# Kernel optimization log

Hardware: AMD Instinct MI355X
Metric: run time of the kernel (lower is better)

Reference implementation:

```python
import jax, jax.numpy as jnp
import numpy as np

N, E, IN_FT, OUT_FT = 8192, 4096, 512, 512
DENSITY = 0.02


def setup_inputs() -> dict:
    key = jax.random.key(0)
    k1, k2, k3, k4 = jax.random.split(key, 4)
    x = jax.random.normal(k1, (N, IN_FT), dtype=jnp.float32)
    hypergraph = (jax.random.uniform(k2, (N, E)) < DENSITY).astype(jnp.float32)
    # kaiming_uniform on [in, out]: fan_in = in_ft (torch fan of a Linear-style 2D param is dim 1 size? torch computes fan_in = size(1) for 2D -> out_ft here)
    bound_w = float(np.sqrt(6.0 / OUT_FT))  # kaiming_uniform a=sqrt(5)? default a=0 -> gain sqrt(2); bound = gain*sqrt(3/fan_in)
    bound_w = float(np.sqrt(2.0) * np.sqrt(3.0 / OUT_FT))
    weight = jax.random.uniform(k3, (IN_FT, OUT_FT), minval=-bound_w, maxval=bound_w, dtype=jnp.float32)
    bound_v = float(np.sqrt(2.0) * np.sqrt(3.0 / 1.0))
    V = jax.random.uniform(k4, (IN_FT, 1), minval=-bound_v, maxval=bound_v, dtype=jnp.float32)
    bias = jnp.zeros((OUT_FT,), dtype=jnp.float32)
    return {"x": x, "hypergraph": hypergraph, "weight": weight, "V": V, "bias": bias}


def reference(x, hypergraph, weight, V, bias):
    # edge embeddings: H^T @ x  -> [E, in_ft]
    edge_emb = hypergraph.T @ x
    hw = jax.nn.sigmoid(edge_emb @ V)          # [E, 1] learned hyperedge weights
    w = hw[:, 0]                                # [E]
    deg_v = (hypergraph @ hw)[:, 0]             # [N]  (sum over last dim of H @ hw)
    deg_e = jnp.sum(hypergraph, axis=0)         # [E]
    # adj = diag(deg_v) @ H @ diag(w) @ diag(deg_e) @ H^T @ diag(deg_v)
    # fused as broadcasted row/col scalings around two GEMMs (same math, no NxN)
    out = x @ weight                            # [N, out_ft]
    t = hypergraph.T @ (deg_v[:, None] * out)   # [E, out_ft]
    t = (w * deg_e)[:, None] * t                # diagonal edge scalings
    out = deg_v[:, None] * (hypergraph @ t)     # [N, out_ft]
    out = out + bias
    return (out, w)
```

## Files before the change

kernel.cpp:

```cpp
#include <hip/hip_runtime.h>


#define N_NODES 8192
#define N_EDGES 4096
#define FT 512

typedef short bf16x8 __attribute__((ext_vector_type(8)));
typedef float f32x4 __attribute__((ext_vector_type(4)));
typedef unsigned short u16;
typedef unsigned int u32;

__device__ __forceinline__ u16 f2b(float f) {
    union { float f; u32 u; } v; v.f = f;
    u32 r = v.u + 0x7FFFu + ((v.u >> 16) & 1u);
    return (u16)(r >> 16);
}
__device__ __forceinline__ float b2f(u16 h) {
    union { u32 u; float f; } v; v.u = ((u32)h) << 16; return v.f;
}


__global__ __launch_bounds__(256) void zero_kernel(float* p, int n) {
    int i = blockIdx.x * 256 + threadIdx.x;
    if (i < n) p[i] = 0.f;
}

__global__ __launch_bounds__(256) void xv_xb_kernel(const float* __restrict__ x,
                                                    const float* __restrict__ V,
                                                    float* __restrict__ xv,
                                                    u16* __restrict__ xb) {
    int row = blockIdx.x * 4 + (threadIdx.x >> 6);
    int lane = threadIdx.x & 63;
    const float* xr = x + (size_t)row * FT + lane * 8;
    const float* vr = V + lane * 8;
    float4 a0 = *(const float4*)xr, a1 = *(const float4*)(xr + 4);
    float4 b0 = *(const float4*)vr, b1 = *(const float4*)(vr + 4);
    float acc = a0.x * b0.x + a0.y * b0.y + a0.z * b0.z + a0.w * b0.w +
                a1.x * b1.x + a1.y * b1.y + a1.z * b1.z + a1.w * b1.w;
    u16 tmp[8] = {f2b(a0.x), f2b(a0.y), f2b(a0.z), f2b(a0.w),
                  f2b(a1.x), f2b(a1.y), f2b(a1.z), f2b(a1.w)};
    *(uint4*)(xb + (size_t)row * FT + lane * 8) = *(uint4*)tmp;
#pragma unroll
    for (int off = 32; off; off >>= 1) acc += __shfl_down(acc, off);
    if (lane == 0) xv[row] = acc;
}

__global__ __launch_bounds__(256) void prep_h2_kernel(const float* __restrict__ H,
                                                      const float* __restrict__ xv,
                                                      u16* __restrict__ Hbf,
                                                      u16* __restrict__ HTbf,
                                                      float* __restrict__ zsum,
                                                      float* __restrict__ desum) {
    __shared__ u32 Wt[64][33];
    __shared__ float xvs[64];
    const int t = threadIdx.x;
    const int e0 = blockIdx.x * 64, n0 = blockIdx.y * 64;
    if (t < 64) xvs[t] = xv[n0 + t];
    {
        int n = t >> 2, seg = t & 3;
        const float* src = H + (size_t)(n0 + n) * N_EDGES + e0 + seg * 16;
        u16* hdst = Hbf + (size_t)(n0 + n) * N_EDGES + e0 + seg * 16;
        u32 o[8];
#pragma unroll
        for (int j = 0; j < 4; j++) {
            float4 h = *(const float4*)(src + j * 4);
            o[2 * j]     = (h.x != 0.f ? 0x3F80u : 0u) | (h.y != 0.f ? 0x3F800000u : 0u);
            o[2 * j + 1] = (h.z != 0.f ? 0x3F80u : 0u) | (h.w != 0.f ? 0x3F800000u : 0u);
        }
        *(uint4*)hdst       = *(uint4*)&o[0];
        *(uint4*)(hdst + 8) = *(uint4*)&o[4];
#pragma unroll
        for (int j = 0; j < 8; j++) Wt[n][seg * 8 + j] = o[j];
    }
    __syncthreads();
    {
        int e = t >> 2, g = t & 3;
        int ew = e >> 1;
        u32 sel = (e & 1) ? 0x07060302u : 0x05040100u;
        u32 oo[8];
        float z = 0.f, d = 0.f;
#pragma unroll
        for (int j = 0; j < 8; j++) {
            int np = g * 8 + j;
            oo[j] = __builtin_amdgcn_perm(Wt[2 * np + 1][ew], Wt[2 * np][ew], sel);
            z += (oo[j] & 0xFFFFu) ? xvs[2 * np] : 0.f;
            d += (oo[j] & 0xFFFFu) ? 1.f : 0.f;
            z += (oo[j] >> 16) ? xvs[2 * np + 1] : 0.f;
            d += (oo[j] >> 16) ? 1.f : 0.f;
        }
        u32* drow = (u32*)(HTbf + (size_t)(e0 + e) * N_NODES + n0);
        *(uint4*)(drow + g * 8)     = *(uint4*)&oo[0];
        *(uint4*)(drow + g * 8 + 4) = *(uint4*)&oo[4];
        z += __shfl_down(z, 2); z += __shfl_down(z, 1);
        d += __shfl_down(d, 2); d += __shfl_down(d, 1);
        if (g == 0) {
            atomicAdd(zsum + e0 + e, z);
            atomicAdd(desum + e0 + e, d);
        }
    }
}

__global__ __launch_bounds__(256) void sigmoid_kernel(const float* __restrict__ zsum,
                                                      const float* __restrict__ desum,
                                                      float* __restrict__ w_out,
                                                      float* __restrict__ wde) {
    int e = blockIdx.x * 256 + threadIdx.x;
    float z = zsum[e];
    float wv = 1.f / (1.f + expf(-z));
    w_out[e] = wv;
    wde[e] = wv * desum[e];
}

__global__ __launch_bounds__(256) void degv_kernel(const u16* __restrict__ Hbf,
                                                   const float* __restrict__ w,
                                                   float* __restrict__ degv) {
    int row = blockIdx.x * 4 + (threadIdx.x >> 6);
    int lane = threadIdx.x & 63;
    const uint4* hr = (const uint4*)(Hbf + (size_t)row * N_EDGES);
    float acc = 0.f;
#pragma unroll
    for (int i = 0; i < 8; i++) {
        int idx = i * 64 + lane;
        uint4 h = hr[idx];
        const float* w8 = w + idx * 8;
        float4 wa = *(const float4*)w8, wb = *(const float4*)(w8 + 4);
        acc += (h.x & 0xFFFFu) ? wa.x : 0.f;  acc += (h.x >> 16) ? wa.y : 0.f;
        acc += (h.y & 0xFFFFu) ? wa.z : 0.f;  acc += (h.y >> 16) ? wa.w : 0.f;
        acc += (h.z & 0xFFFFu) ? wb.x : 0.f;  acc += (h.z >> 16) ? wb.y : 0.f;
        acc += (h.w & 0xFFFFu) ? wb.z : 0.f;  acc += (h.w >> 16) ? wb.w : 0.f;
    }
#pragma unroll
    for (int off = 32; off; off >>= 1) acc += __shfl_down(acc, off);
    if (lane == 0) degv[row] = acc;
}

__global__ void wt_kernel(const float* __restrict__ src, u16* __restrict__ dst) {
    __shared__ float tile[32][33];
    int tx = threadIdx.x, ty = threadIdx.y;
    int c = blockIdx.x * 32 + tx;
    int r0 = blockIdx.y * 32;
#pragma unroll
    for (int i = 0; i < 4; i++)
        tile[ty + i * 8][tx] = src[(size_t)(r0 + ty + i * 8) * FT + c];
    __syncthreads();
#pragma unroll
    for (int i = 0; i < 4; i++)
        dst[(size_t)(blockIdx.x * 32 + ty + i * 8) * FT + r0 + tx] = f2b(tile[tx][ty + i * 8]);
}

__global__ void t2t_kernel(const u16* __restrict__ P, const float* __restrict__ wde,
                           u16* __restrict__ t2T) {
    __shared__ float tile[32][33];
    int tx = threadIdx.x, ty = threadIdx.y;
    int f0 = blockIdx.x * 32, e0 = blockIdx.y * 32;
#pragma unroll
    for (int i = 0; i < 4; i++) {
        int e = e0 + ty + i * 8;
        size_t idx = (size_t)e * 512 + f0 + tx;
        float s = 0.f;
#pragma unroll
        for (int sl = 0; sl < 8; sl++)
            s += b2f(P[idx + (size_t)sl * N_EDGES * 512]);
        tile[ty + i * 8][tx] = wde[e] * s;
    }
    __syncthreads();
#pragma unroll
    for (int i = 0; i < 4; i++)
        t2T[(size_t)(f0 + ty + i * 8) * N_EDGES + e0 + tx] = f2b(tile[tx][ty + i * 8]);
}

__global__ __launch_bounds__(256) void final_kernel(const u16* __restrict__ P,
                                                    const float* __restrict__ degv,
                                                    const float* __restrict__ bias,
                                                    float* __restrict__ out) {
    int i8 = blockIdx.x * 256 + threadIdx.x;
    int base = i8 * 8;
    int n = base >> 9, f = base & 511;
    float s[8] = {0.f, 0.f, 0.f, 0.f, 0.f, 0.f, 0.f, 0.f};
#pragma unroll
    for (int sl = 0; sl < 4; sl++) {
        uint4 v = *(const uint4*)(P + (size_t)sl * N_NODES * 512 + base);
        u32 ws[4] = {v.x, v.y, v.z, v.w};
#pragma unroll
        for (int j = 0; j < 4; j++) {
            s[2 * j]     += b2f((u16)(ws[j] & 0xFFFFu));
            s[2 * j + 1] += b2f((u16)(ws[j] >> 16));
        }
    }
    float dv = degv[n];
    float4 o0, o1;
    o0.x = dv * s[0] + bias[f + 0]; o0.y = dv * s[1] + bias[f + 1];
    o0.z = dv * s[2] + bias[f + 2]; o0.w = dv * s[3] + bias[f + 3];
    o1.x = dv * s[4] + bias[f + 4]; o1.y = dv * s[5] + bias[f + 5];
    o1.z = dv * s[6] + bias[f + 6]; o1.w = dv * s[7] + bias[f + 7];
    *(float4*)(out + base) = o0;
    *(float4*)(out + base + 4) = o1;
}


#define TBK 64

template <int MT, int NT, int EPI>
__global__ __launch_bounds__(256, 4)
void gemm9(const u16* __restrict__ Ap, const u16* __restrict__ Bp,
           void* __restrict__ Cp, const float* __restrict__ degv,
           int KC, int lda, int ldb, int ldc, size_t Ssz) {
    __shared__ __align__(16) u16 Alds[MT * 32 * TBK];
    __shared__ __align__(16) u16 Blds[NT * 32 * TBK];
    const int t = threadIdx.x;
    const int m0 = blockIdx.x * (MT * 32), n0 = blockIdx.y * (NT * 32);
    const int kbase = blockIdx.z * KC;
    const int wave = t >> 6, lane = t & 63, quad = lane >> 4, lo = lane & 15;
    const int wm = (wave >> 1) * (MT * 16), wn = (wave & 1) * (NT * 16);

    f32x4 acc[MT][NT];
#pragma unroll
    for (int a = 0; a < MT; a++)
#pragma unroll
        for (int b = 0; b < NT; b++) acc[a][b] = (f32x4){0.f, 0.f, 0.f, 0.f};

    for (int kk = 0; kk < KC; kk += TBK) {
        const int k0 = kbase + kk;
        __syncthreads();
#pragma unroll
        for (int i = 0; i < MT; i++) {
            int c = t + i * 256;
            int r = c >> 3;
            int j = ((c & 7) - r) & 7;
            const u16* g = Ap + (size_t)(m0 + r) * lda + k0 + j * 8;
            __builtin_amdgcn_global_load_lds((const u32*)g, (u32*)(Alds + c * 8), 16, 0, 0);
        }
#pragma unroll
        for (int i = 0; i < NT; i++) {
            int c = t + i * 256;
            int r = c >> 3;
            int j = ((c & 7) - r) & 7;
            const u16* g = Bp + (size_t)(n0 + r) * ldb + k0 + j * 8;
            __builtin_amdgcn_global_load_lds((const u32*)g, (u32*)(Blds + c * 8), 16, 0, 0);
        }
        __syncthreads();

#pragma unroll
        for (int s2 = 0; s2 < 2; s2++) {
            bf16x8 af[MT], bfr[NT];
#pragma unroll
            for (int mt = 0; mt < MT; mt++) {
                int m = wm + mt * 16 + lo;
                int s = (s2 * 4 + quad + m) & 7;
                af[mt] = *(const bf16x8*)&Alds[m * TBK + s * 8];
            }
#pragma unroll
            for (int nt = 0; nt < NT; nt++) {
                int n = wn + nt * 16 + lo;
                int s = (s2 * 4 + quad + n) & 7;
                bfr[nt] = *(const bf16x8*)&Blds[n * TBK + s * 8];
            }
#pragma unroll
            for (int mt = 0; mt < MT; mt++)
#pragma unroll
                for (int nt = 0; nt < NT; nt++)
                    acc[mt][nt] = __builtin_amdgcn_mfma_f32_16x16x32_bf16(af[mt], bfr[nt], acc[mt][nt], 0, 0, 0);
        }
    }

    if (EPI == 0) {
        u16* C = (u16*)Cp + (size_t)blockIdx.z * Ssz;
#pragma unroll
        for (int mt = 0; mt < MT; mt++) {
            int rb = m0 + wm + mt * 16 + quad * 4;
#pragma unroll
            for (int i = 0; i < 4; i++)
#pragma unroll
                for (int nt = 0; nt < NT; nt++)
                    C[(size_t)(rb + i) * ldc + n0 + wn + nt * 16 + lo] = f2b(acc[mt][nt][i]);
        }
    } else {
        u16* C = (u16*)Cp;
        float dv[NT];
#pragma unroll
        for (int nt = 0; nt < NT; nt++) dv[nt] = degv[n0 + wn + nt * 16 + lo];
#pragma unroll
        for (int mt = 0; mt < MT; mt++) {
            int rb = m0 + wm + mt * 16 + quad * 4;
#pragma unroll
            for (int i = 0; i < 4; i++)
#pragma unroll
                for (int nt = 0; nt < NT; nt++)
                    C[(size_t)(rb + i) * ldc + n0 + wn + nt * 16 + lo] =
                        f2b(acc[mt][nt][i] * dv[nt]);
        }
    }
}


extern "C" void kernel_launch(void* const* d_in, const int* in_sizes, int n_in,
                              void* d_out, int out_size, void* d_ws, size_t ws_size,
                              hipStream_t stream) {
    const float* x    = (const float*)d_in[0];
    const float* H    = (const float*)d_in[1];
    const float* W    = (const float*)d_in[2];
    const float* V    = (const float*)d_in[3];
    const float* bias = (const float*)d_in[4];
    float* out  = (float*)d_out;
    float* wout = out + (size_t)N_NODES * FT;
    (void)in_sizes; (void)n_in; (void)out_size; (void)ws_size;

    char* wsb = (char*)d_ws;
    float* wsf   = (float*)d_ws;
    float* xv    = wsf;
    float* zsum  = wsf + 8192;
    float* desum = wsf + 12288;
    float* degv  = wsf + 16384;
    float* wde   = wsf + 24576;
    u16*   Hbf   = (u16*)(wsb + 114688);
    u16*   HTbf  = (u16*)(wsb + 67223552);
    u16*   WT    = (u16*)(wsb + 134332416);
    u16*   doutT = (u16*)(wsb + 134856704);
    u16*   t2T   = (u16*)(wsb + 143245312);
    u16*   xb    = (u16*)(wsb + 147439616);
    u16*   P     = (u16*)(wsb + 155828224);

    zero_kernel<<<32, 256, 0, stream>>>(zsum, 8192);
    xv_xb_kernel<<<N_NODES / 4, 256, 0, stream>>>(x, V, xv, xb);
    prep_h2_kernel<<<dim3(N_EDGES / 64, N_NODES / 64), 256, 0, stream>>>(
        H, xv, Hbf, HTbf, zsum, desum);
    sigmoid_kernel<<<N_EDGES / 256, 256, 0, stream>>>(zsum, desum, wout, wde);
    degv_kernel<<<N_NODES / 4, 256, 0, stream>>>(Hbf, wout, degv);
    wt_kernel<<<dim3(16, 16), dim3(32, 8), 0, stream>>>(W, WT);

    gemm9<2, 4, 1><<<dim3(FT / 64, N_NODES / 128, 1), 256, 0, stream>>>(
        WT, xb, doutT, degv, FT, FT, FT, N_NODES, 0);

    gemm9<4, 4, 0><<<dim3(N_EDGES / 128, FT / 128, 8), 256, 0, stream>>>(
        HTbf, doutT, P, nullptr, N_NODES / 8, N_NODES, N_NODES, 512, (size_t)N_EDGES * 512);

    t2t_kernel<<<dim3(FT / 32, N_EDGES / 32), dim3(32, 8), 0, stream>>>(P, wde, t2T);

    gemm9<4, 4, 0><<<dim3(N_NODES / 128, FT / 128, 4), 256, 0, stream>>>(
        Hbf, t2T, P, nullptr, N_EDGES / 4, N_EDGES, N_EDGES, 512, (size_t)N_NODES * 512);

    final_kernel<<<(N_NODES * FT / 8) / 256, 256, 0, stream>>>(P, degv, bias, out);
}
```

Measured before the change: 356.1 us.

## Replace dense incidence GEMMs with sparse adjacency-list gather SpMM

Builds per-node and per-edge index lists from the incidence matrix in a single pass, using a wave prefix scan for node lists and atomic slot claims for edge lists. Edge weights, edge degrees and node degrees are then computed by gathering over those lists. The two large dense H^T and H GEMMs, the split-K partial buffers and their reduce kernels are replaced by row-gather SpMM kernels that read bf16 rows of the small projected feature matrices. The x@W GEMM now applies the deg_v row scaling in its epilogue and writes row-major output. Fixed list capacities (160 per node, 256 per edge) silently truncate if the hypergraph is denser than expected, and the atomic-built edge lists have nondeterministic order.

```diff
diff --git a/kernel.cpp b/kernel.cpp
--- a/kernel.cpp
+++ b/kernel.cpp
@@ -4,6 +4,8 @@
 #define N_NODES 8192
 #define N_EDGES 4096
 #define FT 512
+#define NODE_CAP 160
+#define EDGE_CAP 256
 
 typedef short bf16x8 __attribute__((ext_vector_type(8)));
 typedef float f32x4 __attribute__((ext_vector_type(4)));
@@ -20,15 +22,12 @@
 }
 
 
-__global__ __launch_bounds__(256) void zero_kernel(float* p, int n) {
-    int i = blockIdx.x * 256 + threadIdx.x;
-    if (i < n) p[i] = 0.f;
-}
-
 __global__ __launch_bounds__(256) void xv_xb_kernel(const float* __restrict__ x,
                                                     const float* __restrict__ V,
                                                     float* __restrict__ xv,
-                                                    u16* __restrict__ xb) {
+                                                    u16* __restrict__ xb,
+                                                    u32* __restrict__ edge_cnt) {
+    if (blockIdx.x < 16) edge_cnt[blockIdx.x * 256 + threadIdx.x] = 0u;
     int row = blockIdx.x * 4 + (threadIdx.x >> 6);
     int lane = threadIdx.x & 63;
     const float* xr = x + (size_t)row * FT + lane * 8;
@@ -45,93 +44,78 @@
     if (lane == 0) xv[row] = acc;
 }
 
-__global__ __launch_bounds__(256) void prep_h2_kernel(const float* __restrict__ H,
-                                                      const float* __restrict__ xv,
-                                                      u16* __restrict__ Hbf,
-                                                      u16* __restrict__ HTbf,
-                                                      float* __restrict__ zsum,
-                                                      float* __restrict__ desum) {
-    __shared__ u32 Wt[64][33];
-    __shared__ float xvs[64];
-    const int t = threadIdx.x;
-    const int e0 = blockIdx.x * 64, n0 = blockIdx.y * 64;
-    if (t < 64) xvs[t] = xv[n0 + t];
-    {
-        int n = t >> 2, seg = t & 3;
-        const float* src = H + (size_t)(n0 + n) * N_EDGES + e0 + seg * 16;
-        u16* hdst = Hbf + (size_t)(n0 + n) * N_EDGES + e0 + seg * 16;
-        u32 o[8];
+__global__ __launch_bounds__(256) void bld_kernel(const float* __restrict__ H,
+                                                  u16* __restrict__ node_list,
+                                                  u32* __restrict__ node_cnt,
+                                                  u16* __restrict__ edge_list,
+                                                  u32* __restrict__ edge_cnt) {
+    const int n = blockIdx.x * 4 + (threadIdx.x >> 6);
+    const int lane = threadIdx.x & 63;
+    const float4* hrow = (const float4*)(H + (size_t)n * N_EDGES);
+    u16* nl = node_list + (size_t)n * NODE_CAP;
+    int base = 0;
+    for (int chunk = 0; chunk < 16; chunk++) {
+        float4 h = hrow[chunk * 64 + lane];
+        u32 m = (h.x != 0.f ? 1u : 0u) | (h.y != 0.f ? 2u : 0u) |
+                (h.z != 0.f ? 4u : 0u) | (h.w != 0.f ? 8u : 0u);
+        int c = __popc(m);
+        int sc = c;
+#pragma unroll
+        for (int off = 1; off < 64; off <<= 1) {
+            int v = __shfl_up(sc, off);
+            if (lane >= off) sc += v;
+        }
+        int ofs = base + sc - c;
+        int tot = __shfl(sc, 63);
+        int e0 = chunk * 256 + lane * 4;
 #pragma unroll
         for (int j = 0; j < 4; j++) {
-            float4 h = *(const float4*)(src + j * 4);
-            o[2 * j]     = (h.x != 0.f ? 0x3F80u : 0u) | (h.y != 0.f ? 0x3F800000u : 0u);
-            o[2 * j + 1] = (h.z != 0.f ? 0x3F80u : 0u) | (h.w != 0.f ? 0x3F800000u : 0u);
-        }
-        *(uint4*)hdst       = *(uint4*)&o[0];
-        *(uint4*)(hdst + 8) = *(uint4*)&o[4];
-#pragma unroll
-        for (int j = 0; j < 8; j++) Wt[n][seg * 8 + j] = o[j];
-    }
-    __syncthreads();
-    {
-        int e = t >> 2, g = t & 3;
-        int ew = e >> 1;
-        u32 sel = (e & 1) ? 0x07060302u : 0x05040100u;
-        u32 oo[8];
-        float z = 0.f, d = 0.f;
-#pragma unroll
-        for (int j = 0; j < 8; j++) {
-            int np = g * 8 + j;
-            oo[j] = __builtin_amdgcn_perm(Wt[2 * np + 1][ew], Wt[2 * np][ew], sel);
-            z += (oo[j] & 0xFFFFu) ? xvs[2 * np] : 0.f;
-            d += (oo[j] & 0xFFFFu) ? 1.f : 0.f;
-            z += (oo[j] >> 16) ? xvs[2 * np + 1] : 0.f;
-            d += (oo[j] >> 16) ? 1.f : 0.f;
-        }
-        u32* drow = (u32*)(HTbf + (size_t)(e0 + e) * N_NODES + n0);
-        *(uint4*)(drow + g * 8)     = *(uint4*)&oo[0];
-        *(uint4*)(drow + g * 8 + 4) = *(uint4*)&oo[4];
-        z += __shfl_down(z, 2); z += __shfl_down(z, 1);
-        d += __shfl_down(d, 2); d += __shfl_down(d, 1);
-        if (g == 0) {
-            atomicAdd(zsum + e0 + e, z);
-            atomicAdd(desum + e0 + e, d);
-        }
-    }
-}
-
-__global__ __launch_bounds__(256) void sigmoid_kernel(const float* __restrict__ zsum,
-                                                      const float* __restrict__ desum,
-                                                      float* __restrict__ w_out,
-                                                      float* __restrict__ wde) {
-    int e = blockIdx.x * 256 + threadIdx.x;
-    float z = zsum[e];
-    float wv = 1.f / (1.f + expf(-z));
-    w_out[e] = wv;
-    wde[e] = wv * desum[e];
-}
-
-__global__ __launch_bounds__(256) void degv_kernel(const u16* __restrict__ Hbf,
-                                                   const float* __restrict__ w,
-                                                   float* __restrict__ degv) {
-    int row = blockIdx.x * 4 + (threadIdx.x >> 6);
+            if (m & (1u << j)) {
+                int e = e0 + j;
+                if (ofs < NODE_CAP) nl[ofs] = (u16)e;
+                ofs++;
+                u32 pos = atomicAdd(&edge_cnt[e], 1u);
+                if (pos < EDGE_CAP) edge_list[(size_t)e * EDGE_CAP + pos] = (u16)n;
+            }
+        }
+        base += tot;
+    }
+    if (lane == 0) node_cnt[n] = (u32)(base < NODE_CAP ? base : NODE_CAP);
+}
+
+__global__ __launch_bounds__(256) void zde_kernel(const u16* __restrict__ edge_list,
+                                                  const u32* __restrict__ edge_cnt,
+                                                  const float* __restrict__ xv,
+                                                  float* __restrict__ w_out,
+                                                  float* __restrict__ wde) {
+    int e = blockIdx.x * 4 + (threadIdx.x >> 6);
     int lane = threadIdx.x & 63;
-    const uint4* hr = (const uint4*)(Hbf + (size_t)row * N_EDGES);
+    int cnt = (int)edge_cnt[e]; if (cnt > EDGE_CAP) cnt = EDGE_CAP;
+    const u16* el = edge_list + (size_t)e * EDGE_CAP;
+    float z = 0.f;
+    for (int i = lane; i < cnt; i += 64) z += xv[el[i]];
+#pragma unroll
+    for (int off = 32; off; off >>= 1) z += __shfl_down(z, off);
+    if (lane == 0) {
+        float wv = 1.f / (1.f + expf(-z));
+        w_out[e] = wv;
+        wde[e] = wv * (float)cnt;
+    }
+}
+
+__global__ __launch_bounds__(256) void degv2_kernel(const u16* __restrict__ node_list,
+                                                    const u32* __restrict__ node_cnt,
+                                                    const float* __restrict__ w,
+                                                    float* __restrict__ degv) {
+    int n = blockIdx.x * 4 + (threadIdx.x >> 6);
+    int lane = threadIdx.x & 63;
+    int cnt = (int)node_cnt[n];
+    const u16* nl = node_list + (size_t)n * NODE_CAP;
     float acc = 0.f;
-#pragma unroll
-    for (int i = 0; i < 8; i++) {
-        int idx = i * 64 + lane;
-        uint4 h = hr[idx];
-        const float* w8 = w + idx * 8;
-        float4 wa = *(const float4*)w8, wb = *(const float4*)(w8 + 4);
-        acc += (h.x & 0xFFFFu) ? wa.x : 0.f;  acc += (h.x >> 16) ? wa.y : 0.f;
-        acc += (h.y & 0xFFFFu) ? wa.z : 0.f;  acc += (h.y >> 16) ? wa.w : 0.f;
-        acc += (h.z & 0xFFFFu) ? wb.x : 0.f;  acc += (h.z >> 16) ? wb.y : 0.f;
-        acc += (h.w & 0xFFFFu) ? wb.z : 0.f;  acc += (h.w >> 16) ? wb.w : 0.f;
-    }
+    for (int i = lane; i < cnt; i += 64) acc += w[nl[i]];
 #pragma unroll
     for (int off = 32; off; off >>= 1) acc += __shfl_down(acc, off);
-    if (lane == 0) degv[row] = acc;
+    if (lane == 0) degv[n] = acc;
 }
 
 __global__ void wt_kernel(const float* __restrict__ src, u16* __restrict__ dst) {
@@ -148,53 +132,69 @@
         dst[(size_t)(blockIdx.x * 32 + ty + i * 8) * FT + r0 + tx] = f2b(tile[tx][ty + i * 8]);
 }
 
-__global__ void t2t_kernel(const u16* __restrict__ P, const float* __restrict__ wde,
-                           u16* __restrict__ t2T) {
-    __shared__ float tile[32][33];
-    int tx = threadIdx.x, ty = threadIdx.y;
-    int f0 = blockIdx.x * 32, e0 = blockIdx.y * 32;
-#pragma unroll
-    for (int i = 0; i < 4; i++) {
-        int e = e0 + ty + i * 8;
-        size_t idx = (size_t)e * 512 + f0 + tx;
-        float s = 0.f;
-#pragma unroll
-        for (int sl = 0; sl < 8; sl++)
-            s += b2f(P[idx + (size_t)sl * N_EDGES * 512]);
-        tile[ty + i * 8][tx] = wde[e] * s;
-    }
-    __syncthreads();
-#pragma unroll
-    for (int i = 0; i < 4; i++)
-        t2T[(size_t)(f0 + ty + i * 8) * N_EDGES + e0 + tx] = f2b(tile[tx][ty + i * 8]);
-}
-
-__global__ __launch_bounds__(256) void final_kernel(const u16* __restrict__ P,
+__global__ __launch_bounds__(256) void spmm1_kernel(const u16* __restrict__ edge_list,
+                                                    const u32* __restrict__ edge_cnt,
+                                                    const u16* __restrict__ dout,
+                                                    const float* __restrict__ wde,
+                                                    u16* __restrict__ t2) {
+    const int e = blockIdx.x;
+    const int tid = threadIdx.x;
+    int cnt = (int)edge_cnt[e]; if (cnt > EDGE_CAP) cnt = EDGE_CAP;
+    const u16* el = edge_list + (size_t)e * EDGE_CAP;
+    float a0 = 0.f, a1 = 0.f;
+    int i = 0;
+    for (; i + 4 <= cnt; i += 4) {
+        int n0 = el[i + 0], n1 = el[i + 1], n2 = el[i + 2], n3 = el[i + 3];
+        u32 v0 = *(const u32*)(dout + (size_t)n0 * FT + tid * 2);
+        u32 v1 = *(const u32*)(dout + (size_t)n1 * FT + tid * 2);
+        u32 v2 = *(const u32*)(dout + (size_t)n2 * FT + tid * 2);
+        u32 v3 = *(const u32*)(dout + (size_t)n3 * FT + tid * 2);
+        a0 += b2f((u16)(v0 & 0xFFFFu)); a1 += b2f((u16)(v0 >> 16));
+        a0 += b2f((u16)(v1 & 0xFFFFu)); a1 += b2f((u16)(v1 >> 16));
+        a0 += b2f((u16)(v2 & 0xFFFFu)); a1 += b2f((u16)(v2 >> 16));
+        a0 += b2f((u16)(v3 & 0xFFFFu)); a1 += b2f((u16)(v3 >> 16));
+    }
+    for (; i < cnt; i++) {
+        u32 v = *(const u32*)(dout + (size_t)el[i] * FT + tid * 2);
+        a0 += b2f((u16)(v & 0xFFFFu)); a1 += b2f((u16)(v >> 16));
+    }
+    float s = wde[e];
+    u32 o = (u32)f2b(s * a0) | ((u32)f2b(s * a1) << 16);
+    *(u32*)(t2 + (size_t)e * FT + tid * 2) = o;
+}
+
+__global__ __launch_bounds__(256) void spmm2_kernel(const u16* __restrict__ node_list,
+                                                    const u32* __restrict__ node_cnt,
+                                                    const u16* __restrict__ t2,
                                                     const float* __restrict__ degv,
                                                     const float* __restrict__ bias,
                                                     float* __restrict__ out) {
-    int i8 = blockIdx.x * 256 + threadIdx.x;
-    int base = i8 * 8;
-    int n = base >> 9, f = base & 511;
-    float s[8] = {0.f, 0.f, 0.f, 0.f, 0.f, 0.f, 0.f, 0.f};
-#pragma unroll
-    for (int sl = 0; sl < 4; sl++) {
-        uint4 v = *(const uint4*)(P + (size_t)sl * N_NODES * 512 + base);
-        u32 ws[4] = {v.x, v.y, v.z, v.w};
-#pragma unroll
-        for (int j = 0; j < 4; j++) {
-            s[2 * j]     += b2f((u16)(ws[j] & 0xFFFFu));
-            s[2 * j + 1] += b2f((u16)(ws[j] >> 16));
-        }
+    const int n = blockIdx.x;
+    const int tid = threadIdx.x;
+    int cnt = (int)node_cnt[n];
+    const u16* nl = node_list + (size_t)n * NODE_CAP;
+    float a0 = 0.f, a1 = 0.f;
+    int i = 0;
+    for (; i + 4 <= cnt; i += 4) {
+        int e0 = nl[i + 0], e1 = nl[i + 1], e2 = nl[i + 2], e3 = nl[i + 3];
+        u32 v0 = *(const u32*)(t2 + (size_t)e0 * FT + tid * 2);
+        u32 v1 = *(const u32*)(t2 + (size_t)e1 * FT + tid * 2);
+        u32 v2 = *(const u32*)(t2 + (size_t)e2 * FT + tid * 2);
+        u32 v3 = *(const u32*)(t2 + (size_t)e3 * FT + tid * 2);
+        a0 += b2f((u16)(v0 & 0xFFFFu)); a1 += b2f((u16)(v0 >> 16));
+        a0 += b2f((u16)(v1 & 0xFFFFu)); a1 += b2f((u16)(v1 >> 16));
+        a0 += b2f((u16)(v2 & 0xFFFFu)); a1 += b2f((u16)(v2 >> 16));
+        a0 += b2f((u16)(v3 & 0xFFFFu)); a1 += b2f((u16)(v3 >> 16));
+    }
+    for (; i < cnt; i++) {
+        u32 v = *(const u32*)(t2 + (size_t)nl[i] * FT + tid * 2);
+        a0 += b2f((u16)(v & 0xFFFFu)); a1 += b2f((u16)(v >> 16));
     }
     float dv = degv[n];
-    float4 o0, o1;
-    o0.x = dv * s[0] + bias[f + 0]; o0.y = dv * s[1] + bias[f + 1];
-    o0.z = dv * s[2] + bias[f + 2]; o0.w = dv * s[3] + bias[f + 3];
-    o1.x = dv * s[4] + bias[f + 4]; o1.y = dv * s[5] + bias[f + 5];
-    o1.z = dv * s[6] + bias[f + 6]; o1.w = dv * s[7] + bias[f + 7];
-    *(float4*)(out + base) = o0;
-    *(float4*)(out + base + 4) = o1;
+    float2 o;
+    o.x = dv * a0 + bias[tid * 2 + 0];
+    o.y = dv * a1 + bias[tid * 2 + 1];
+    *(float2*)(out + (size_t)n * FT + tid * 2) = o;
 }
 
 
@@ -204,12 +204,11 @@
 __global__ __launch_bounds__(256, 4)
 void gemm9(const u16* __restrict__ Ap, const u16* __restrict__ Bp,
            void* __restrict__ Cp, const float* __restrict__ degv,
-           int KC, int lda, int ldb, int ldc, size_t Ssz) {
+           int KC, int lda, int ldb, int ldc) {
     __shared__ __align__(16) u16 Alds[MT * 32 * TBK];
     __shared__ __align__(16) u16 Blds[NT * 32 * TBK];
     const int t = threadIdx.x;
     const int m0 = blockIdx.x * (MT * 32), n0 = blockIdx.y * (NT * 32);
-    const int kbase = blockIdx.z * KC;
     const int wave = t >> 6, lane = t & 63, quad = lane >> 4, lo = lane & 15;
     const int wm = (wave >> 1) * (MT * 16), wn = (wave & 1) * (NT * 16);
 
@@ -220,14 +219,13 @@
         for (int b = 0; b < NT; b++) acc[a][b] = (f32x4){0.f, 0.f, 0.f, 0.f};
 
     for (int kk = 0; kk < KC; kk += TBK) {
-        const int k0 = kbase + kk;
         __syncthreads();
 #pragma unroll
         for (int i = 0; i < MT; i++) {
             int c = t + i * 256;
             int r = c >> 3;
             int j = ((c & 7) - r) & 7;
-            const u16* g = Ap + (size_t)(m0 + r) * lda + k0 + j * 8;
+            const u16* g = Ap + (size_t)(m0 + r) * lda + kk + j * 8;
             __builtin_amdgcn_global_load_lds((const u32*)g, (u32*)(Alds + c * 8), 16, 0, 0);
         }
 #pragma unroll
@@ -235,7 +233,7 @@
             int c = t + i * 256;
             int r = c >> 3;
             int j = ((c & 7) - r) & 7;
-            const u16* g = Bp + (size_t)(n0 + r) * ldb + k0 + j * 8;
+            const u16* g = Bp + (size_t)(n0 + r) * ldb + kk + j * 8;
             __builtin_amdgcn_global_load_lds((const u32*)g, (u32*)(Blds + c * 8), 16, 0, 0);
         }
         __syncthreads();
@@ -263,31 +261,19 @@
         }
     }
 
-    if (EPI == 0) {
-        u16* C = (u16*)Cp + (size_t)blockIdx.z * Ssz;
+    if (EPI == 3) {
+        u16* C = (u16*)Cp;
 #pragma unroll
         for (int mt = 0; mt < MT; mt++) {
             int rb = m0 + wm + mt * 16 + quad * 4;
 #pragma unroll
-            for (int i = 0; i < 4; i++)
-#pragma unroll
-                for (int nt = 0; nt < NT; nt++)
-                    C[(size_t)(rb + i) * ldc + n0 + wn + nt * 16 + lo] = f2b(acc[mt][nt][i]);
-        }
-    } else {
-        u16* C = (u16*)Cp;
-        float dv[NT];
-#pragma unroll
-        for (int nt = 0; nt < NT; nt++) dv[nt] = degv[n0 + wn + nt * 16 + lo];
-#pragma unroll
-        for (int mt = 0; mt < MT; mt++) {
-            int rb = m0 + wm + mt * 16 + quad * 4;
-#pragma unroll
-            for (int i = 0; i < 4; i++)
+            for (int i = 0; i < 4; i++) {
+                float dvv = degv[rb + i];
 #pragma unroll
                 for (int nt = 0; nt < NT; nt++)
                     C[(size_t)(rb + i) * ldc + n0 + wn + nt * 16 + lo] =
-                        f2b(acc[mt][nt][i] * dv[nt]);
+                        f2b(acc[mt][nt][i] * dvv);
+            }
         }
     }
 }
@@ -306,38 +292,25 @@
     (void)in_sizes; (void)n_in; (void)out_size; (void)ws_size;
 
     char* wsb = (char*)d_ws;
-    float* wsf   = (float*)d_ws;
-    float* xv    = wsf;
-    float* zsum  = wsf + 8192;
-    float* desum = wsf + 12288;
-    float* degv  = wsf + 16384;
-    float* wde   = wsf + 24576;
-    u16*   Hbf   = (u16*)(wsb + 114688);
-    u16*   HTbf  = (u16*)(wsb + 67223552);
-    u16*   WT    = (u16*)(wsb + 134332416);
-    u16*   doutT = (u16*)(wsb + 134856704);
-    u16*   t2T   = (u16*)(wsb + 143245312);
-    u16*   xb    = (u16*)(wsb + 147439616);
-    u16*   P     = (u16*)(wsb + 155828224);
-
-    zero_kernel<<<32, 256, 0, stream>>>(zsum, 8192);
-    xv_xb_kernel<<<N_NODES / 4, 256, 0, stream>>>(x, V, xv, xb);
-    prep_h2_kernel<<<dim3(N_EDGES / 64, N_NODES / 64), 256, 0, stream>>>(
-        H, xv, Hbf, HTbf, zsum, desum);
-    sigmoid_kernel<<<N_EDGES / 256, 256, 0, stream>>>(zsum, desum, wout, wde);
-    degv_kernel<<<N_NODES / 4, 256, 0, stream>>>(Hbf, wout, degv);
+    float* xv        = (float*)(wsb + 0);
+    float* degv      = (float*)(wsb + 32768);
+    float* wde       = (float*)(wsb + 65536);
+    u32*   edge_cnt  = (u32*)  (wsb + 81920);
+    u32*   node_cnt  = (u32*)  (wsb + 98304);
+    u16*   edge_list = (u16*)  (wsb + 131072);
+    u16*   node_list = (u16*)  (wsb + 2228224);
+    u16*   WT        = (u16*)  (wsb + 4849664);
+    u16*   xb        = (u16*)  (wsb + 5373952);
+    u16*   dout      = (u16*)  (wsb + 13762560);
+    u16*   t2        = (u16*)  (wsb + 22151168);
+
+    xv_xb_kernel<<<N_NODES / 4, 256, 0, stream>>>(x, V, xv, xb, edge_cnt);
+    bld_kernel<<<N_NODES / 4, 256, 0, stream>>>(H, node_list, node_cnt, edge_list, edge_cnt);
+    zde_kernel<<<N_EDGES / 4, 256, 0, stream>>>(edge_list, edge_cnt, xv, wout, wde);
+    degv2_kernel<<<N_NODES / 4, 256, 0, stream>>>(node_list, node_cnt, wout, degv);
     wt_kernel<<<dim3(16, 16), dim3(32, 8), 0, stream>>>(W, WT);
-
-    gemm9<2, 4, 1><<<dim3(FT / 64, N_NODES / 128, 1), 256, 0, stream>>>(
-        WT, xb, doutT, degv, FT, FT, FT, N_NODES, 0);
-
-    gemm9<4, 4, 0><<<dim3(N_EDGES / 128, FT / 128, 8), 256, 0, stream>>>(
-        HTbf, doutT, P, nullptr, N_NODES / 8, N_NODES, N_NODES, 512, (size_t)N_EDGES * 512);
-
-    t2t_kernel<<<dim3(FT / 32, N_EDGES / 32), dim3(32, 8), 0, stream>>>(P, wde, t2T);
-
-    gemm9<4, 4, 0><<<dim3(N_NODES / 128, FT / 128, 4), 256, 0, stream>>>(
-        Hbf, t2T, P, nullptr, N_EDGES / 4, N_EDGES, N_EDGES, 512, (size_t)N_NODES * 512);
-
-    final_kernel<<<(N_NODES * FT / 8) / 256, 256, 0, stream>>>(P, degv, bias, out);
-}
+    gemm9<2, 4, 3><<<dim3(N_NODES / 64, FT / 128, 1), 256, 0, stream>>>(
+        xb, WT, dout, degv, FT, FT, FT, FT);
+    spmm1_kernel<<<N_EDGES, 256, 0, stream>>>(edge_list, edge_cnt, dout, wde, t2);
+    spmm2_kernel<<<N_NODES, 256, 0, stream>>>(node_list, node_cnt, t2, degv, bias, out);
+}
```

After: 487.8 us. 37.0% more time.
